# Performance work log

Hardware: AMD Instinct MI355X
Metric: run time of the kernel (lower is better)

Reference implementation:

```python
import jax, jax.numpy as jnp
import numpy as np

B, N, M = 2, 131072, 512
VOXEL_SIZE = 0.5
SCALE = 10.0          # points lie in [0, SCALE)^3
G = 20                # static voxels per axis: ceil(SCALE / VOXEL_SIZE)
V = G * G * G         # total voxels per batch element


def setup_inputs() -> dict:
    key = jax.random.key(0)
    kx, ks = jax.random.split(key)
    x = jax.random.uniform(kx, (B, N, 3), dtype=jnp.float32) * SCALE
    # random_sample_point_cloud: sample M point indices without replacement per batch
    perm = jax.vmap(lambda k: jax.random.permutation(k, N))(jax.random.split(ks, B))
    sampled_idx = perm[:, :M].astype(jnp.int32)
    return {"x": x, "sampled_idx": sampled_idx}


def _voxel_idx(pts, min_coords):
    # metric_to_voxel_space: floor((p - min) / voxel_size), clipped to the grid
    idx = jnp.floor((pts - min_coords[:, None, :]) / VOXEL_SIZE).astype(jnp.int32)
    return jnp.clip(idx, 0, G - 1)  # (B, n, 3)


def reference(x, sampled_idx):
    # --- estimate_normal_distributions_with_size: per-voxel mean + covariance ---
    min_coords = x.min(axis=1)                                     # (B, 3)
    vox = _voxel_idx(x, min_coords)                                # (B, N, 3)
    flat = (vox[..., 0] * G + vox[..., 1]) * G + vox[..., 2]       # (B, N) flat voxel id

    seg = (flat + jnp.arange(B, dtype=flat.dtype)[:, None] * V).reshape(-1)  # global seg ids
    pts = x.reshape(-1, 3)
    cnt = jax.ops.segment_sum(jnp.ones((B * N,), jnp.float32), seg,
                              num_segments=B * V).reshape(B, V, 1)
    s1 = jax.ops.segment_sum(pts, seg, num_segments=B * V).reshape(B, V, 3)
    outer = (pts[:, :, None] * pts[:, None, :]).reshape(-1, 9)
    s2 = jax.ops.segment_sum(outer, seg, num_segments=B * V).reshape(B, V, 9)

    safe = jnp.maximum(cnt, 1.0)                                   # empty voxels -> zeros
    mean = s1 / safe                                               # (B, V, 3)
    cov = s2 / safe - (mean[:, :, :, None] * mean[:, :, None, :]).reshape(B, V, 9)
    dists = jnp.concatenate([mean, cov], axis=-1)                  # (B, V, 12)

    # --- gather distributions at the sampled points' voxels ---
    sflat = jnp.take_along_axis(flat, sampled_idx.astype(jnp.int32), axis=1)   # (B, M)
    filtered = jnp.take_along_axis(dists, sflat[..., None], axis=1)            # (B, M, 12)
    return filtered
```

## Files before the change

kernel.cpp:

```cpp
#include <hip/hip_runtime.h>

#define BB 2
#define NN 131072
#define MM 512
#define GG 20
#define VV (GG * GG * GG)
#define NBLKX 128

#define OFF_PARTIAL 0
#define OFF_MINV    3072
#define OFF_SFLAT   3200
#define OFF_FLAGS   8192
#define OFF_SUMS    24576
#define ZWORDS      ((16384 + 640000) / 4)

__device__ __forceinline__ int vox_coord(float p, float mn) {
    int i = (int)floorf((p - mn) * 2.0f);
    return min(max(i, 0), GG - 1);
}

__global__ __launch_bounds__(256) void vox_min(const float* __restrict__ x,
                                               char* __restrict__ ws) {
    const int b = blockIdx.y;
    const int tid = blockIdx.x * 256 + threadIdx.x;
    const int gtid = (b * NBLKX + blockIdx.x) * 256 + threadIdx.x;

    {
        int* z = (int*)(ws + OFF_FLAGS);
        for (int i = gtid; i < ZWORDS; i += NBLKX * BB * 256) z[i] = 0;
    }

    const float4* xb = (const float4*)(x + (size_t)b * NN * 3);
    float4 f0 = xb[3 * tid + 0];
    float4 f1 = xb[3 * tid + 1];
    float4 f2 = xb[3 * tid + 2];
    float mx = fminf(fminf(f0.x, f0.w), fminf(f1.z, f2.y));
    float my = fminf(fminf(f0.y, f1.x), fminf(f1.w, f2.z));
    float mz = fminf(fminf(f0.z, f1.y), fminf(f2.x, f2.w));

    for (int off = 32; off > 0; off >>= 1) {
        mx = fminf(mx, __shfl_down(mx, off, 64));
        my = fminf(my, __shfl_down(my, off, 64));
        mz = fminf(mz, __shfl_down(mz, off, 64));
    }
    __shared__ float lmin[4][3];
    int wave = threadIdx.x >> 6;
    if ((threadIdx.x & 63) == 0) {
        lmin[wave][0] = mx; lmin[wave][1] = my; lmin[wave][2] = mz;
    }
    __syncthreads();
    if (threadIdx.x == 0) {
        float* pm = (float*)(ws + OFF_PARTIAL) + (b * NBLKX + blockIdx.x) * 3;
        pm[0] = fminf(fminf(lmin[0][0], lmin[1][0]), fminf(lmin[2][0], lmin[3][0]));
        pm[1] = fminf(fminf(lmin[0][1], lmin[1][1]), fminf(lmin[2][1], lmin[3][1]));
        pm[2] = fminf(fminf(lmin[0][2], lmin[1][2]), fminf(lmin[2][2], lmin[3][2]));
    }
}

__global__ __launch_bounds__(1024) void vox_mark(const float* __restrict__ x,
                                                 const int* __restrict__ sidx,
                                                 char* __restrict__ ws) {
    __shared__ float smin[BB][3];
    const int t = threadIdx.x;

    if (t < 384) {
        int pair = t >> 6;
        int lane = t & 63;
        int pb = pair / 3, axis = pair % 3;
        const float* pm = (const float*)(ws + OFF_PARTIAL);
        float m = fminf(pm[(pb * NBLKX + lane) * 3 + axis],
                        pm[(pb * NBLKX + lane + 64) * 3 + axis]);
        for (int off = 32; off > 0; off >>= 1)
            m = fminf(m, __shfl_down(m, off, 64));
        if (lane == 0) {
            smin[pb][axis] = m;
            ((float*)(ws + OFF_MINV))[pb * 3 + axis] = m;
        }
    }
    __syncthreads();

    int b = t >> 9;
    int pi = sidx[t];
    const float* p = x + ((size_t)b * NN + pi) * 3;
    int ix = vox_coord(p[0], smin[b][0]);
    int iy = vox_coord(p[1], smin[b][1]);
    int iz = vox_coord(p[2], smin[b][2]);
    int flat = (ix * GG + iy) * GG + iz;
    ((int*)(ws + OFF_SFLAT))[t] = flat;
    ((unsigned char*)(ws + OFF_FLAGS))[b * VV + flat] = 1;
}

__global__ __launch_bounds__(256) void vox_accum(const float* __restrict__ x,
                                                 char* __restrict__ ws) {
    const int b = blockIdx.y;
    const int tid = blockIdx.x * 256 + threadIdx.x;
    const float* mv = (const float*)(ws + OFF_MINV) + b * 3;
    const float mnx = mv[0], mny = mv[1], mnz = mv[2];
    const unsigned char* flags = (const unsigned char*)(ws + OFF_FLAGS) + b * VV;
    float* sums = (float*)(ws + OFF_SUMS) + (size_t)b * VV * 10;

    const float4* xb = (const float4*)(x + (size_t)b * NN * 3);
    float4 f0 = xb[3 * tid + 0];
    float4 f1 = xb[3 * tid + 1];
    float4 f2 = xb[3 * tid + 2];
    float px[4] = {f0.x, f0.w, f1.z, f2.y};
    float py[4] = {f0.y, f1.x, f1.w, f2.z};
    float pz[4] = {f0.z, f1.y, f2.x, f2.w};
#pragma unroll
    for (int k = 0; k < 4; ++k) {
        int ix = vox_coord(px[k], mnx);
        int iy = vox_coord(py[k], mny);
        int iz = vox_coord(pz[k], mnz);
        int flat = (ix * GG + iy) * GG + iz;
        if (flags[flat]) {
            float* s = sums + (size_t)flat * 10;
            unsafeAtomicAdd(s + 0, 1.0f);
            unsafeAtomicAdd(s + 1, px[k]);
            unsafeAtomicAdd(s + 2, py[k]);
            unsafeAtomicAdd(s + 3, pz[k]);
            unsafeAtomicAdd(s + 4, px[k] * px[k]);
            unsafeAtomicAdd(s + 5, px[k] * py[k]);
            unsafeAtomicAdd(s + 6, px[k] * pz[k]);
            unsafeAtomicAdd(s + 7, py[k] * py[k]);
            unsafeAtomicAdd(s + 8, py[k] * pz[k]);
            unsafeAtomicAdd(s + 9, pz[k] * pz[k]);
        }
    }
}

__global__ __launch_bounds__(256) void vox_final(const char* __restrict__ ws,
                                                 float* __restrict__ out) {
    int t = blockIdx.x * 256 + threadIdx.x;
    if (t >= BB * MM) return;
    int b = t >> 9;
    int flat = ((const int*)(ws + OFF_SFLAT))[t];
    const float* s = (const float*)(ws + OFF_SUMS) + ((size_t)b * VV + flat) * 10;
    float cnt = s[0];
    float inv = 1.0f / fmaxf(cnt, 1.0f);
    float mx = s[1] * inv, my = s[2] * inv, mz = s[3] * inv;
    float cxx = s[4] * inv - mx * mx;
    float cxy = s[5] * inv - mx * my;
    float cxz = s[6] * inv - mx * mz;
    float cyy = s[7] * inv - my * my;
    float cyz = s[8] * inv - my * mz;
    float czz = s[9] * inv - mz * mz;
    float* o = out + (size_t)t * 12;
    o[0] = mx;  o[1] = my;  o[2] = mz;
    o[3] = cxx; o[4] = cxy; o[5] = cxz;
    o[6] = cxy; o[7] = cyy; o[8] = cyz;
    o[9] = cxz; o[10] = cyz; o[11] = czz;
}

extern "C" void kernel_launch(void* const* d_in, const int* in_sizes, int n_in,
                              void* d_out, int out_size, void* d_ws, size_t ws_size,
                              hipStream_t stream) {
    const float* x = (const float*)d_in[0];
    const int* sidx = (const int*)d_in[1];
    float* out = (float*)d_out;
    char* ws = (char*)d_ws;

    vox_min<<<dim3(NBLKX, BB), 256, 0, stream>>>(x, ws);
    vox_mark<<<1, 1024, 0, stream>>>(x, sidx, ws);
    vox_accum<<<dim3(NBLKX, BB), 256, 0, stream>>>(x, ws);
    vox_final<<<(BB * MM + 255) / 256, 256, 0, stream>>>(ws, out);
}
```

Measured before the change: 80.35 us.

## Fuse mark kernel into accumulate via per-block LDS bitmap of sampled voxels

Removes the single-block mark kernel. Each accumulate block now redundantly reduces the per-axis minimum and builds an LDS bitmap of the sampled voxels, which replaces the global byte-flag array. The final kernel recomputes the sampled voxel ids itself, and zeroing uses int4 stores sized to the sums buffer only. This cuts one launch and a serial single-block stage, at the cost of every block repeating the min reduction and the 512 sampled-point gathers.

```diff
diff --git a/kernel.cpp b/kernel.cpp
--- a/kernel.cpp
+++ b/kernel.cpp
@@ -8,15 +8,25 @@
 #define NBLKX 128
 
 #define OFF_PARTIAL 0
-#define OFF_MINV    3072
-#define OFF_SFLAT   3200
-#define OFF_FLAGS   8192
-#define OFF_SUMS    24576
-#define ZWORDS      ((16384 + 640000) / 4)
+#define OFF_SUMS    4096
+#define ZI4         (640000 / 16)
 
 __device__ __forceinline__ int vox_coord(float p, float mn) {
     int i = (int)floorf((p - mn) * 2.0f);
     return min(max(i, 0), GG - 1);
+}
+
+__device__ __forceinline__ void reduce_min_prologue(const char* ws, int b, int t,
+                                                    float* smin) {
+    if (t < 192) {
+        const int axis = t >> 6, lane = t & 63;
+        const float* pm = (const float*)(ws + OFF_PARTIAL);
+        float m = fminf(pm[(b * NBLKX + lane) * 3 + axis],
+                        pm[(b * NBLKX + lane + 64) * 3 + axis]);
+        for (int off = 32; off > 0; off >>= 1)
+            m = fminf(m, __shfl_down(m, off, 64));
+        if (lane == 0) smin[axis] = m;
+    }
 }
 
 __global__ __launch_bounds__(256) void vox_min(const float* __restrict__ x,
@@ -26,8 +36,8 @@
     const int gtid = (b * NBLKX + blockIdx.x) * 256 + threadIdx.x;
 
     {
-        int* z = (int*)(ws + OFF_FLAGS);
-        for (int i = gtid; i < ZWORDS; i += NBLKX * BB * 256) z[i] = 0;
+        int4* z = (int4*)(ws + OFF_SUMS);
+        if (gtid < ZI4) z[gtid] = make_int4(0, 0, 0, 0);
     }
 
     const float4* xb = (const float4*)(x + (size_t)b * NN * 3);
@@ -57,48 +67,35 @@
     }
 }
 
-__global__ __launch_bounds__(1024) void vox_mark(const float* __restrict__ x,
+__global__ __launch_bounds__(256) void vox_accum(const float* __restrict__ x,
                                                  const int* __restrict__ sidx,
                                                  char* __restrict__ ws) {
-    __shared__ float smin[BB][3];
+    const int b = blockIdx.y;
     const int t = threadIdx.x;
+    const int tid = blockIdx.x * 256 + t;
 
-    if (t < 384) {
-        int pair = t >> 6;
-        int lane = t & 63;
-        int pb = pair / 3, axis = pair % 3;
-        const float* pm = (const float*)(ws + OFF_PARTIAL);
-        float m = fminf(pm[(pb * NBLKX + lane) * 3 + axis],
-                        pm[(pb * NBLKX + lane + 64) * 3 + axis]);
-        for (int off = 32; off > 0; off >>= 1)
-            m = fminf(m, __shfl_down(m, off, 64));
-        if (lane == 0) {
-            smin[pb][axis] = m;
-            ((float*)(ws + OFF_MINV))[pb * 3 + axis] = m;
-        }
+    __shared__ float smin[3];
+    __shared__ unsigned int bm[250];
+
+    if (t < 250) bm[t] = 0u;
+    reduce_min_prologue(ws, b, t, smin);
+    __syncthreads();
+    const float mnx = smin[0], mny = smin[1], mnz = smin[2];
+
+#pragma unroll
+    for (int k = 0; k < 2; ++k) {
+        const int j = t + k * 256;
+        const int pi = sidx[b * MM + j];
+        const float* p = x + ((size_t)b * NN + pi) * 3;
+        int ix = vox_coord(p[0], mnx);
+        int iy = vox_coord(p[1], mny);
+        int iz = vox_coord(p[2], mnz);
+        int flat = (ix * GG + iy) * GG + iz;
+        atomicOr(&bm[flat >> 5], 1u << (flat & 31));
     }
     __syncthreads();
 
-    int b = t >> 9;
-    int pi = sidx[t];
-    const float* p = x + ((size_t)b * NN + pi) * 3;
-    int ix = vox_coord(p[0], smin[b][0]);
-    int iy = vox_coord(p[1], smin[b][1]);
-    int iz = vox_coord(p[2], smin[b][2]);
-    int flat = (ix * GG + iy) * GG + iz;
-    ((int*)(ws + OFF_SFLAT))[t] = flat;
-    ((unsigned char*)(ws + OFF_FLAGS))[b * VV + flat] = 1;
-}
-
-__global__ __launch_bounds__(256) void vox_accum(const float* __restrict__ x,
-                                                 char* __restrict__ ws) {
-    const int b = blockIdx.y;
-    const int tid = blockIdx.x * 256 + threadIdx.x;
-    const float* mv = (const float*)(ws + OFF_MINV) + b * 3;
-    const float mnx = mv[0], mny = mv[1], mnz = mv[2];
-    const unsigned char* flags = (const unsigned char*)(ws + OFF_FLAGS) + b * VV;
     float* sums = (float*)(ws + OFF_SUMS) + (size_t)b * VV * 10;
-
     const float4* xb = (const float4*)(x + (size_t)b * NN * 3);
     float4 f0 = xb[3 * tid + 0];
     float4 f1 = xb[3 * tid + 1];
@@ -112,7 +109,7 @@
         int iy = vox_coord(py[k], mny);
         int iz = vox_coord(pz[k], mnz);
         int flat = (ix * GG + iy) * GG + iz;
-        if (flags[flat]) {
+        if ((bm[flat >> 5] >> (flat & 31)) & 1u) {
             float* s = sums + (size_t)flat * 10;
             unsafeAtomicAdd(s + 0, 1.0f);
             unsafeAtomicAdd(s + 1, px[k]);
@@ -128,12 +125,24 @@
     }
 }
 
-__global__ __launch_bounds__(256) void vox_final(const char* __restrict__ ws,
+__global__ __launch_bounds__(512) void vox_final(const float* __restrict__ x,
+                                                 const int* __restrict__ sidx,
+                                                 const char* __restrict__ ws,
                                                  float* __restrict__ out) {
-    int t = blockIdx.x * 256 + threadIdx.x;
-    if (t >= BB * MM) return;
-    int b = t >> 9;
-    int flat = ((const int*)(ws + OFF_SFLAT))[t];
+    const int b = blockIdx.x;
+    const int t = threadIdx.x;
+
+    __shared__ float smin[3];
+    reduce_min_prologue(ws, b, t, smin);
+    __syncthreads();
+
+    const int pi = sidx[b * MM + t];
+    const float* p = x + ((size_t)b * NN + pi) * 3;
+    int ix = vox_coord(p[0], smin[0]);
+    int iy = vox_coord(p[1], smin[1]);
+    int iz = vox_coord(p[2], smin[2]);
+    int flat = (ix * GG + iy) * GG + iz;
+
     const float* s = (const float*)(ws + OFF_SUMS) + ((size_t)b * VV + flat) * 10;
     float cnt = s[0];
     float inv = 1.0f / fmaxf(cnt, 1.0f);
@@ -144,7 +153,7 @@
     float cyy = s[7] * inv - my * my;
     float cyz = s[8] * inv - my * mz;
     float czz = s[9] * inv - mz * mz;
-    float* o = out + (size_t)t * 12;
+    float* o = out + (size_t)(b * MM + t) * 12;
     o[0] = mx;  o[1] = my;  o[2] = mz;
     o[3] = cxx; o[4] = cxy; o[5] = cxz;
     o[6] = cxy; o[7] = cyy; o[8] = cyz;
@@ -160,7 +169,6 @@
     char* ws = (char*)d_ws;
 
     vox_min<<<dim3(NBLKX, BB), 256, 0, stream>>>(x, ws);
-    vox_mark<<<1, 1024, 0, stream>>>(x, sidx, ws);
-    vox_accum<<<dim3(NBLKX, BB), 256, 0, stream>>>(x, ws);
-    vox_final<<<(BB * MM + 255) / 256, 256, 0, stream>>>(ws, out);
+    vox_accum<<<dim3(NBLKX, BB), 256, 0, stream>>>(x, sidx, ws);
+    vox_final<<<BB, 512, 0, stream>>>(x, sidx, ws, out);
 }
```

Result: faster. 77.65 us (median of 2 runs) (-3.4%).
